# Kernel tuning notes

Measured on AMD Instinct MI355X. Metric: run time of the kernel, lower is better.

## Reference

```python
import jax, jax.numpy as jnp
import numpy as np

D_OUT = 32


def mlp(x, Ws, bs):
    # Ws: (L+1, d, d), bs: (L+1, d); relu after hidden layers, linear output
    h = x
    n = Ws.shape[0]
    for i in range(n - 1):
        h = jax.nn.relu(h @ Ws[i] + bs[i])
    return h @ Ws[n - 1] + bs[n - 1]


def causal_dot_product(Q, K, V, t1, t2):
    """out[:,:,i] = Q_i @ sum_{j: t2[j] <= t1[i]} K_j V_j^T.
    t2 is sorted (timestamps), so the cumulative outer-product state can be
    computed with a cumsum and gathered via searchsorted.
    Q: (1,1,T1,d); K,V: (1,1,T2,d); t1: (T1,); t2: (T2,).
    """
    outer = K[..., :, :, None] * V[..., :, None, :]      # (1,1,T2,d,d)
    S = jnp.cumsum(outer, axis=2)                        # prefix states
    idx = jnp.searchsorted(t2, t1, side='right') - 1     # (T1,)
    valid = idx >= 0
    Sg = S[:, :, jnp.maximum(idx, 0)]                    # (1,1,T1,d,d)
    out = jnp.einsum('bhid,bhide->bhie', Q, Sg)
    return jnp.where(valid[None, None, :, None], out, jnp.zeros((), out.dtype))


def _with_sorted_time(x, key):
    T = x.shape[2]
    t = jnp.sort(jax.random.uniform(key, (T,), dtype=jnp.float32)) * 100.0
    return x.at[0, 0, :, -1].set(t)


def setup_inputs() -> dict:
    key = jax.random.key(0)
    ks = jax.random.split(key, 16)
    d = 64
    Ts = [4096, 6144, 8192, 4096]
    mods = {}
    for i, T in enumerate(Ts):
        x = jax.random.normal(ks[i], (1, 1, T, d), dtype=jnp.float32)
        mods[f'm{i+1}'] = _with_sorted_time(x, ks[8 + i])
    scale = 1.0 / np.sqrt(d)
    WQ_w = jax.random.normal(ks[4], (3, d, d), dtype=jnp.float32) * scale
    WQ_b = jnp.zeros((3, d), dtype=jnp.float32)
    WK_w = jax.random.normal(ks[5], (4, 3, d, d), dtype=jnp.float32) * scale
    WK_b = jnp.zeros((4, 3, d), dtype=jnp.float32)
    return dict(m1=mods['m1'], m2=mods['m2'], m3=mods['m3'], m4=mods['m4'],
                WQ_w=WQ_w, WQ_b=WQ_b, WK_w=WK_w, WK_b=WK_b)


def reference(m1, m2, m3, m4, WQ_w, WQ_b, WK_w, WK_b):
    Q = mlp(m1, WQ_w, WQ_b)            # (1,1,T1,d)
    t1 = m1[0, 0, :, -1]               # (T1,)
    total = None
    for mi, X in enumerate([m1, m2, m3, m4]):
        K = mlp(X, WK_w[mi], WK_b[mi])
        V = X
        t2 = X[0, 0, :, -1]
        Z = causal_dot_product(Q, K, V, t1, t2)  # (1,1,T1,d)
        total = Z if total is None else total + Z
    # cat over dim=1 then sum(1) == sum of per-modality results, dim 1 dropped
    yhat = total.sum(axis=1)[..., :D_OUT]        # (1,T1,d_out)
    return yhat
```

## Files before the change

kernel.cpp:

```cpp
#include <hip/hip_runtime.h>


#define QB_OFF   0
#define KB_OFF   131072
#define SP_OFF   851968
#define TD_OFF   1581056
#define C_OFF    1603584

typedef __attribute__((ext_vector_type(8))) short short8;
typedef __attribute__((ext_vector_type(4))) float floatx4;

__device__ __forceinline__ unsigned short f2bf(float f) {
    union { float f; unsigned u; } v; v.f = f;
    unsigned r = v.u + 0x7fff + ((v.u >> 16) & 1);
    return (unsigned short)(r >> 16);
}

#define MFMA16(a,b,c) __builtin_amdgcn_mfma_f32_16x16x32_bf16((a),(b),(c),0,0,0)

__global__ __launch_bounds__(256) void k_fused(
    const float* __restrict__ x0, const float* __restrict__ x1,
    const float* __restrict__ x2, const float* __restrict__ x3,
    const float* __restrict__ wq_w, const float* __restrict__ wq_b,
    const float* __restrict__ wk_w, const float* __restrict__ wk_b,
    float* __restrict__ ws)
{
    __shared__ unsigned short H0[64*72];
    __shared__ unsigned short H1[64*72];
    __shared__ unsigned short Wt[3][64*72];
    __shared__ unsigned short KT[64*72];
    __shared__ unsigned short VT[32*72];

    const int tid = threadIdx.x;
    const int bid = blockIdx.x;

    int task, rb;
    if (bid < 64)       { task = 0; rb = bid; }
    else if (bid < 128) { task = 1; rb = bid - 64; }
    else if (bid < 224) { task = 2; rb = bid - 128; }
    else if (bid < 352) { task = 3; rb = bid - 224; }
    else                { task = 4; rb = bid - 352; }

    const float* Xs[4] = {x0, x1, x2, x3};
    const int rowoff[4] = {0, 4096, 10240, 18432};
    const int spoff[4]  = {0, 65, 162, 291};

    const float* X; const float* W; const float* Bv; int mm = -1;
    if (task == 0) { X = x0; W = wq_w; Bv = wq_b; }
    else {
        mm = task - 1;
        X = Xs[mm]; W = wk_w + mm*3*64*64; Bv = wk_b + mm*3*64;
    }

    const int row0 = rb * 64;

    {
        const float4* X4 = (const float4*)(X + (size_t)row0*64);
        #pragma unroll
        for (int k = 0; k < 4; ++k) {
            int idx = k*256 + tid;
            float4 v = X4[idx];
            int rr = idx >> 4, c4 = (idx & 15) * 4;
            ushort4 h;
            h.x = f2bf(v.x); h.y = f2bf(v.y); h.z = f2bf(v.z); h.w = f2bf(v.w);
            *(ushort4*)&H0[rr*72 + c4] = h;
        }
        const float4* W4 = (const float4*)W;
        #pragma unroll
        for (int k = 0; k < 12; ++k) {
            int idx = k*256 + tid;
            float4 v = W4[idx];
            int l = idx >> 10, rest = idx & 1023;
            int d = rest >> 4, c4 = (rest & 15) * 4;
            Wt[l][(c4+0)*72 + d] = f2bf(v.x);
            Wt[l][(c4+1)*72 + d] = f2bf(v.y);
            Wt[l][(c4+2)*72 + d] = f2bf(v.z);
            Wt[l][(c4+3)*72 + d] = f2bf(v.w);
        }
    }
    if (task > 0 && tid < 64)
        ws[TD_OFF + rowoff[mm] + row0 + tid] = X[(size_t)(row0 + tid)*64 + 63];
    __syncthreads();

    const int w    = tid >> 6;
    const int lane = tid & 63;
    const int lm   = lane & 15;
    const int q    = lane >> 4;
    const int col  = w*16 + lm;

    #pragma unroll 1
    for (int l = 0; l < 3; ++l) {
        const unsigned short* Hin  = (l & 1) ? H1 : H0;
        unsigned short*       Hout = (l & 1) ? H0 : H1;
        float bias = Bv[l*64 + col];
        short8 b0 = *(const short8*)&Wt[l][col*72 + q*8];
        short8 b1 = *(const short8*)&Wt[l][col*72 + 32 + q*8];
        #pragma unroll
        for (int mt = 0; mt < 4; ++mt) {
            floatx4 acc = {bias, bias, bias, bias};
            short8 a0 = *(const short8*)&Hin[(mt*16+lm)*72 + q*8];
            short8 a1 = *(const short8*)&Hin[(mt*16+lm)*72 + 32 + q*8];
            acc = MFMA16(a0, b0, acc);
            acc = MFMA16(a1, b1, acc);
            int r0 = mt*16 + q*4;
            #pragma unroll
            for (int r = 0; r < 4; ++r) {
                float f = acc[r];
                if (l < 2) f = fmaxf(f, 0.0f);
                unsigned short hb = f2bf(f);
                Hout[(r0+r)*72 + col] = hb;
                if (l == 2 && task > 0) KT[col*72 + r0 + r] = hb;
            }
        }
        __syncthreads();
    }

    {
        unsigned short* dst = (task == 0)
            ? (unsigned short*)(ws + QB_OFF)
            : (unsigned short*)(ws + KB_OFF) + (size_t)rowoff[mm]*64;
        #pragma unroll
        for (int k = 0; k < 4; ++k) {
            int idx = k*256 + tid;
            int rr = idx >> 4, c4 = (idx & 15) * 4;
            *(ushort4*)&dst[(size_t)(row0 + rr)*64 + c4] = *(ushort4*)&H1[rr*72 + c4];
        }
    }
    if (task == 0) return;

    {
        #pragma unroll
        for (int k = 0; k < 2; ++k) {
            int idx = k*256 + tid;
            int j = idx >> 3, e4 = (idx & 7) * 4;
            float4 v = *(const float4*)&X[(size_t)(row0 + j)*64 + e4];
            VT[(e4+0)*72 + j] = f2bf(v.x);
            VT[(e4+1)*72 + j] = f2bf(v.y);
            VT[(e4+2)*72 + j] = f2bf(v.z);
            VT[(e4+3)*72 + j] = f2bf(v.w);
        }
    }
    float* spbase = ws + SP_OFF + (size_t)spoff[mm]*2048;
    if (rb == 0)
        for (int idx = tid; idx < 2048; idx += 256) spbase[idx] = 0.0f;
    __syncthreads();

    {
        float* slot = spbase + (size_t)(rb + 1) * 2048;
        #pragma unroll
        for (int nt = 0; nt < 2; ++nt) {
            floatx4 acc = {0.f, 0.f, 0.f, 0.f};
            #pragma unroll
            for (int ks = 0; ks < 2; ++ks) {
                short8 aa = *(const short8*)&KT[col*72 + ks*32 + q*8];
                short8 bb = *(const short8*)&VT[(nt*16+lm)*72 + ks*32 + q*8];
                acc = MFMA16(aa, bb, acc);
            }
            #pragma unroll
            for (int r = 0; r < 4; ++r)
                slot[(w*16 + q*4 + r)*32 + nt*16 + lm] = acc[r];
        }
    }
}

__global__ __launch_bounds__(256) void k_prefix(float* __restrict__ ws,
                                                float* __restrict__ out)
{
    const int nslots[4] = {65, 97, 129, 65};
    const int spoff[4]  = {0, 65, 162, 291};
    const int Tm[4]     = {4096, 6144, 8192, 4096};
    const int rowoff[4] = {0, 4096, 10240, 18432};
    const int bid = blockIdx.x;
    const int tid = threadIdx.x;

    if (bid < 32) {
        int chain = bid*256 + tid;
        int m = chain >> 11, entry = chain & 2047;
        float* p = ws + SP_OFF + (size_t)spoff[m]*2048 + entry;
        const int n = nslots[m];
        float s = 0.0f;
        #pragma unroll 8
        for (int k = 0; k < n; ++k) {
            float v = p[(size_t)k*2048];
            s += v;
            p[(size_t)k*2048] = s;
        }
    } else if (bid < 34) {
        const float* td = ws + TD_OFF;
        int* ctab = (int*)(ws + C_OFF);
        int g = (bid - 32)*256 + tid;
        int m = g >> 7, tile = (g >> 1) & 63, bound = g & 1;
        float t = td[tile*64 + (bound ? 63 : 0)];
        const float* t2 = td + rowoff[m];
        int lo = 0, hi = Tm[m];
        while (lo < hi) {
            int mid = (lo + hi) >> 1;
            if (t2[mid] <= t) lo = mid + 1; else hi = mid;
        }
        ctab[g] = lo;
    } else {
        float4 z = make_float4(0.f, 0.f, 0.f, 0.f);
        #pragma unroll
        for (int k = 0; k < 16; ++k)
            ((float4*)out)[(bid - 34)*4096 + k*256 + tid] = z;
    }
}

__global__ __launch_bounds__(256) void k_query(
    const float* __restrict__ x0, const float* __restrict__ x1,
    const float* __restrict__ x2, const float* __restrict__ x3,
    float* __restrict__ ws, float* __restrict__ out)
{
    __shared__ unsigned short qs[64*72];
    __shared__ unsigned short kc[64*72];
    __shared__ unsigned short vt[32*72];
    __shared__ unsigned short st[32*72];
    __shared__ unsigned short ps[64*72];
    __shared__ float tq[64];
    __shared__ float tcs[64];

    const int tid  = threadIdx.x;
    const int m    = blockIdx.x & 3;
    const int tile = (blockIdx.x >> 2) & 63;
    const int slot = blockIdx.x >> 8;
    const int i0   = tile * 64;

    const float* Xs[4] = {x0, x1, x2, x3};
    const int rowoff[4] = {0, 4096, 10240, 18432};
    const int spoff[4]  = {0, 65, 162, 291};
    const float* X = Xs[m];

    const int* ctab = (const int*)(ws + C_OFF);
    const int c_lo = ctab[m*128 + tile*2 + 0];
    const int c_hi = ctab[m*128 + tile*2 + 1];
    const int B0   = c_lo >> 6;
    const int Bhi  = (c_hi + 63) >> 6;

    if (slot == 1 && B0 + 1 >= Bhi) return;

    const unsigned short* Qg = (const unsigned short*)(ws + QB_OFF);
    const unsigned short* Kg = (const unsigned short*)(ws + KB_OFF) + (size_t)rowoff[m]*64;
    const float* td = ws + TD_OFF;
    const float* sp = ws + SP_OFF + (size_t)(spoff[m] + B0)*2048;

    #pragma unroll
    for (int k = 0; k < 4; ++k) {
        int idx = k*256 + tid;
        int rr = idx >> 4, c4 = (idx & 15) * 4;
        *(ushort4*)&qs[rr*72 + c4] = *(const ushort4*)&Qg[(size_t)(i0 + rr)*64 + c4];
    }
    if (slot == 0) {
        #pragma unroll
        for (int k = 0; k < 8; ++k) {
            int idx = k*256 + tid;
            int d = idx >> 5, e = idx & 31;
            st[e*72 + d] = f2bf(sp[idx]);
        }
    }
    if (tid < 64) tq[tid] = td[i0 + tid];
    __syncthreads();

    const int w    = tid >> 6;
    const int lane = tid & 63;
    const int lm   = lane & 15;
    const int q    = lane >> 4;

    float t1v[16];
    #pragma unroll
    for (int mt = 0; mt < 4; ++mt)
        #pragma unroll
        for (int r = 0; r < 4; ++r)
            t1v[mt*4 + r] = tq[mt*16 + q*4 + r];

    short8 qa[4][2];
    #pragma unroll
    for (int mt = 0; mt < 4; ++mt) {
        qa[mt][0] = *(const short8*)&qs[(mt*16+lm)*72 + q*8];
        qa[mt][1] = *(const short8*)&qs[(mt*16+lm)*72 + 32 + q*8];
    }

    floatx4 accO[2];
    accO[0] = (floatx4){0.f, 0.f, 0.f, 0.f};
    accO[1] = (floatx4){0.f, 0.f, 0.f, 0.f};

    if (slot == 0) {
        #pragma unroll
        for (int nt = 0; nt < 2; ++nt) {
            #pragma unroll
            for (int ks = 0; ks < 2; ++ks) {
                short8 b = *(const short8*)&st[(nt*16+lm)*72 + ks*32 + q*8];
                accO[nt] = MFMA16(qa[w][ks], b, accO[nt]);
            }
        }
    }

    #pragma unroll 1
    for (int B = B0 + slot; B < Bhi; B += 2) {
        __syncthreads();
        #pragma unroll
        for (int k = 0; k < 4; ++k) {
            int idx = k*256 + tid;
            int j = idx >> 4, c4 = (idx & 15) * 4;
            *(ushort4*)&kc[j*72 + c4] = *(const ushort4*)&Kg[(size_t)(B*64 + j)*64 + c4];
        }
        #pragma unroll
        for (int k = 0; k < 2; ++k) {
            int idx = k*256 + tid;
            int j = idx >> 3, e4 = (idx & 7) * 4;
            float4 v = *(const float4*)&X[(size_t)(B*64 + j)*64 + e4];
            vt[(e4+0)*72 + j] = f2bf(v.x);
            vt[(e4+1)*72 + j] = f2bf(v.y);
            vt[(e4+2)*72 + j] = f2bf(v.z);
            vt[(e4+3)*72 + j] = f2bf(v.w);
        }
        if (tid < 64) tcs[tid] = td[rowoff[m] + B*64 + tid];
        __syncthreads();

        {
            short8 bk0 = *(const short8*)&kc[(w*16+lm)*72 + q*8];
            short8 bk1 = *(const short8*)&kc[(w*16+lm)*72 + 32 + q*8];
            float t2j = tcs[w*16 + lm];
            #pragma unroll
            for (int mt = 0; mt < 4; ++mt) {
                floatx4 f = {0.f, 0.f, 0.f, 0.f};
                f = MFMA16(qa[mt][0], bk0, f);
                f = MFMA16(qa[mt][1], bk1, f);
                #pragma unroll
                for (int r = 0; r < 4; ++r) {
                    float p = (t2j <= t1v[mt*4 + r]) ? f[r] : 0.0f;
                    ps[(mt*16 + q*4 + r)*72 + w*16 + lm] = f2bf(p);
                }
            }
        }
        __syncthreads();

        {
            short8 pa0 = *(const short8*)&ps[(w*16+lm)*72 + q*8];
            short8 pa1 = *(const short8*)&ps[(w*16+lm)*72 + 32 + q*8];
            #pragma unroll
            for (int nt = 0; nt < 2; ++nt) {
                short8 bv0 = *(const short8*)&vt[(nt*16+lm)*72 + q*8];
                short8 bv1 = *(const short8*)&vt[(nt*16+lm)*72 + 32 + q*8];
                accO[nt] = MFMA16(pa0, bv0, accO[nt]);
                accO[nt] = MFMA16(pa1, bv1, accO[nt]);
            }
        }
    }

    #pragma unroll
    for (int nt = 0; nt < 2; ++nt)
        #pragma unroll
        for (int r = 0; r < 4; ++r) {
            int i = w*16 + q*4 + r;
            int e = nt*16 + lm;
            atomicAdd(&out[(size_t)(i0 + i)*32 + e], accO[nt][r]);
        }
}

extern "C" void kernel_launch(void* const* d_in, const int* in_sizes, int n_in,
                              void* d_out, int out_size, void* d_ws, size_t ws_size,
                              hipStream_t stream) {
    const float* x0   = (const float*)d_in[0];
    const float* x1   = (const float*)d_in[1];
    const float* x2   = (const float*)d_in[2];
    const float* x3   = (const float*)d_in[3];
    const float* wq_w = (const float*)d_in[4];
    const float* wq_b = (const float*)d_in[5];
    const float* wk_w = (const float*)d_in[6];
    const float* wk_b = (const float*)d_in[7];
    float* ws  = (float*)d_ws;
    float* out = (float*)d_out;

    hipLaunchKernelGGL(k_fused,  dim3(416), dim3(256), 0, stream,
                       x0, x1, x2, x3, wq_w, wq_b, wk_w, wk_b, ws);
    hipLaunchKernelGGL(k_prefix, dim3(42),  dim3(256), 0, stream, ws, out);
    hipLaunchKernelGGL(k_query,  dim3(512), dim3(256), 0, stream,
                       x0, x1, x2, x3, ws, out);
}
```

Measured before the change: 107.3 us.

## Merge three kernels into one cooperative persistent kernel with grid syncs

Replaces the three separate launches (MLP plus chunk states, prefix scan, query) with a single cooperative kernel of 416 blocks that uses grid-wide syncs between phases. Work is redistributed: the prefix scan runs on 128 blocks split into quarters, the boundary search on two blocks, and the query tiles are looped over the persistent grid. This is meant to remove kernel launch gaps and tail effects between phases, at the cost of grid-sync overhead and a loop where 512 tiles over 416 blocks may leave load imbalance. It falls back to the old three-kernel path if the cooperative launch fails.

```diff
diff --git a/kernel.cpp b/kernel.cpp
--- a/kernel.cpp
+++ b/kernel.cpp
@@ -1,4 +1,7 @@
 #include <hip/hip_runtime.h>
+#include <hip/hip_cooperative_groups.h>
+
+namespace cg = cooperative_groups;
 
 
 #define QB_OFF   0
@@ -17,6 +20,344 @@
 }
 
 #define MFMA16(a,b,c) __builtin_amdgcn_mfma_f32_16x16x32_bf16((a),(b),(c),0,0,0)
+
+__global__ __launch_bounds__(256, 2) void k_all(
+    const float* __restrict__ x0, const float* __restrict__ x1,
+    const float* __restrict__ x2, const float* __restrict__ x3,
+    const float* __restrict__ wq_w, const float* __restrict__ wq_b,
+    const float* __restrict__ wk_w, const float* __restrict__ wk_b,
+    float* __restrict__ ws, float* __restrict__ out)
+{
+    __shared__ unsigned short SH[6*4608 + 2304];
+    __shared__ float SF[320];
+
+    const int tid = threadIdx.x;
+    const int bid = blockIdx.x;
+
+    const float* Xs[4] = {x0, x1, x2, x3};
+    const int rowoff[4] = {0, 4096, 10240, 18432};
+    const int spoff[4]  = {0, 65, 162, 291};
+    const int nslots[4] = {65, 97, 129, 65};
+    const int Tm[4]     = {4096, 6144, 8192, 4096};
+
+    const int w    = tid >> 6;
+    const int lane = tid & 63;
+    const int lm   = lane & 15;
+    const int q    = lane >> 4;
+    const int col  = w*16 + lm;
+
+    {
+        unsigned short* H0 = SH;
+        unsigned short* H1 = SH + 4608;
+        unsigned short* Wt = SH + 2*4608;
+        unsigned short* KT = SH + 5*4608;
+        unsigned short* VT = SH + 6*4608;
+
+        int task, rb;
+        if (bid < 64)       { task = 0; rb = bid; }
+        else if (bid < 128) { task = 1; rb = bid - 64; }
+        else if (bid < 224) { task = 2; rb = bid - 128; }
+        else if (bid < 352) { task = 3; rb = bid - 224; }
+        else                { task = 4; rb = bid - 352; }
+
+        const float* X; const float* W; const float* Bv; int mm = -1;
+        if (task == 0) { X = x0; W = wq_w; Bv = wq_b; }
+        else {
+            mm = task - 1;
+            X = Xs[mm]; W = wk_w + mm*3*64*64; Bv = wk_b + mm*3*64;
+        }
+
+        const int row0 = rb * 64;
+
+        {
+            const float4* X4 = (const float4*)(X + (size_t)row0*64);
+            #pragma unroll
+            for (int k = 0; k < 4; ++k) {
+                int idx = k*256 + tid;
+                float4 v = X4[idx];
+                int rr = idx >> 4, c4 = (idx & 15) * 4;
+                ushort4 h;
+                h.x = f2bf(v.x); h.y = f2bf(v.y); h.z = f2bf(v.z); h.w = f2bf(v.w);
+                *(ushort4*)&H0[rr*72 + c4] = h;
+            }
+            const float4* W4 = (const float4*)W;
+            #pragma unroll
+            for (int k = 0; k < 12; ++k) {
+                int idx = k*256 + tid;
+                float4 v = W4[idx];
+                int l = idx >> 10, rest = idx & 1023;
+                int d = rest >> 4, c4 = (rest & 15) * 4;
+                Wt[l*4608 + (c4+0)*72 + d] = f2bf(v.x);
+                Wt[l*4608 + (c4+1)*72 + d] = f2bf(v.y);
+                Wt[l*4608 + (c4+2)*72 + d] = f2bf(v.z);
+                Wt[l*4608 + (c4+3)*72 + d] = f2bf(v.w);
+            }
+        }
+        if (task == 0) {
+            float4 z = make_float4(0.f, 0.f, 0.f, 0.f);
+            ((float4*)out)[bid*512 + tid] = z;
+            ((float4*)out)[bid*512 + 256 + tid] = z;
+        }
+        if (task > 0 && tid < 64)
+            ws[TD_OFF + rowoff[mm] + row0 + tid] = X[(size_t)(row0 + tid)*64 + 63];
+        __syncthreads();
+
+        #pragma unroll 1
+        for (int l = 0; l < 3; ++l) {
+            const unsigned short* Hin  = (l & 1) ? H1 : H0;
+            unsigned short*       Hout = (l & 1) ? H0 : H1;
+            float bias = Bv[l*64 + col];
+            short8 b0 = *(const short8*)&Wt[l*4608 + col*72 + q*8];
+            short8 b1 = *(const short8*)&Wt[l*4608 + col*72 + 32 + q*8];
+            #pragma unroll
+            for (int mt = 0; mt < 4; ++mt) {
+                floatx4 acc = {bias, bias, bias, bias};
+                short8 a0 = *(const short8*)&Hin[(mt*16+lm)*72 + q*8];
+                short8 a1 = *(const short8*)&Hin[(mt*16+lm)*72 + 32 + q*8];
+                acc = MFMA16(a0, b0, acc);
+                acc = MFMA16(a1, b1, acc);
+                int r0 = mt*16 + q*4;
+                #pragma unroll
+                for (int r = 0; r < 4; ++r) {
+                    float f = acc[r];
+                    if (l < 2) f = fmaxf(f, 0.0f);
+                    unsigned short hb = f2bf(f);
+                    Hout[(r0+r)*72 + col] = hb;
+                    if (l == 2 && task > 0) KT[col*72 + r0 + r] = hb;
+                }
+            }
+            __syncthreads();
+        }
+
+        {
+            unsigned short* dst = (task == 0)
+                ? (unsigned short*)(ws + QB_OFF)
+                : (unsigned short*)(ws + KB_OFF) + (size_t)rowoff[mm]*64;
+            #pragma unroll
+            for (int k = 0; k < 4; ++k) {
+                int idx = k*256 + tid;
+                int rr = idx >> 4, c4 = (idx & 15) * 4;
+                *(ushort4*)&dst[(size_t)(row0 + rr)*64 + c4] = *(ushort4*)&H1[rr*72 + c4];
+            }
+        }
+
+        if (task > 0) {
+            #pragma unroll
+            for (int k = 0; k < 2; ++k) {
+                int idx = k*256 + tid;
+                int j = idx >> 3, e4 = (idx & 7) * 4;
+                float4 v = *(const float4*)&X[(size_t)(row0 + j)*64 + e4];
+                VT[(e4+0)*72 + j] = f2bf(v.x);
+                VT[(e4+1)*72 + j] = f2bf(v.y);
+                VT[(e4+2)*72 + j] = f2bf(v.z);
+                VT[(e4+3)*72 + j] = f2bf(v.w);
+            }
+            float* spbase = ws + SP_OFF + (size_t)spoff[mm]*2048;
+            if (rb == 0)
+                for (int idx = tid; idx < 2048; idx += 256) spbase[idx] = 0.0f;
+            __syncthreads();
+
+            float* slot = spbase + (size_t)(rb + 1) * 2048;
+            #pragma unroll
+            for (int nt = 0; nt < 2; ++nt) {
+                floatx4 acc = {0.f, 0.f, 0.f, 0.f};
+                #pragma unroll
+                for (int ks = 0; ks < 2; ++ks) {
+                    short8 aa = *(const short8*)&KT[col*72 + ks*32 + q*8];
+                    short8 bb = *(const short8*)&VT[(nt*16+lm)*72 + ks*32 + q*8];
+                    acc = MFMA16(aa, bb, acc);
+                }
+                #pragma unroll
+                for (int r = 0; r < 4; ++r)
+                    slot[(w*16 + q*4 + r)*32 + nt*16 + lm] = acc[r];
+            }
+        }
+    }
+
+    __threadfence();
+    cg::this_grid().sync();
+
+    if (bid < 128) {
+        const int m   = bid >> 5;
+        const int e   = tid & 63;
+        const int qtr = tid >> 6;
+        const int entry = (bid & 31)*64 + e;
+        const int n = nslots[m];
+        float* p = ws + SP_OFF + (size_t)spoff[m]*2048 + entry;
+        const int k0 = (qtr*n) >> 2;
+        const int k1 = ((qtr+1)*n) >> 2;
+        float s = 0.0f;
+        #pragma unroll 8
+        for (int k = k0; k < k1; ++k) s += p[(size_t)k*2048];
+        SF[qtr*64 + e] = s;
+        __syncthreads();
+        float base = 0.0f;
+        #pragma unroll
+        for (int q2 = 0; q2 < 3; ++q2) if (q2 < qtr) base += SF[q2*64 + e];
+        s = base;
+        #pragma unroll 8
+        for (int k = k0; k < k1; ++k) {
+            s += p[(size_t)k*2048];
+            p[(size_t)k*2048] = s;
+        }
+    } else if (bid < 130) {
+        const float* td = ws + TD_OFF;
+        int* ctab = (int*)(ws + C_OFF);
+        int g = (bid - 128)*256 + tid;
+        int m = g >> 7, tile = (g >> 1) & 63, bound = g & 1;
+        float t = td[tile*64 + (bound ? 63 : 0)];
+        const float* t2 = td + rowoff[m];
+        int lo = 0, hi = Tm[m];
+        while (lo < hi) {
+            int mid = (lo + hi) >> 1;
+            if (t2[mid] <= t) lo = mid + 1; else hi = mid;
+        }
+        ctab[g] = lo;
+    }
+
+    __threadfence();
+    cg::this_grid().sync();
+
+    {
+        unsigned short* qs = SH;
+        unsigned short* kc = SH + 4608;
+        unsigned short* ps = SH + 2*4608;
+        unsigned short* vt = SH + 3*4608;
+        unsigned short* st = SH + 3*4608 + 2304;
+        float* tq  = SF;
+        float* tcs = SF + 64;
+
+        for (int lb = bid; lb < 512; lb += 416) {
+            __syncthreads();
+            const int m    = lb & 3;
+            const int tile = (lb >> 2) & 63;
+            const int slot = lb >> 8;
+            const int i0   = tile * 64;
+            const float* X = Xs[m];
+
+            const int* ctab = (const int*)(ws + C_OFF);
+            const int c_lo = ctab[m*128 + tile*2 + 0];
+            const int c_hi = ctab[m*128 + tile*2 + 1];
+            const int B0   = c_lo >> 6;
+            const int Bhi  = (c_hi + 63) >> 6;
+
+            if (slot == 1 && B0 + 1 >= Bhi) continue;
+
+            const unsigned short* Qg = (const unsigned short*)(ws + QB_OFF);
+            const unsigned short* Kg = (const unsigned short*)(ws + KB_OFF) + (size_t)rowoff[m]*64;
+            const float* td = ws + TD_OFF;
+            const float* sp = ws + SP_OFF + (size_t)(spoff[m] + B0)*2048;
+
+            #pragma unroll
+            for (int k = 0; k < 4; ++k) {
+                int idx = k*256 + tid;
+                int rr = idx >> 4, c4 = (idx & 15) * 4;
+                *(ushort4*)&qs[rr*72 + c4] = *(const ushort4*)&Qg[(size_t)(i0 + rr)*64 + c4];
+            }
+            if (slot == 0) {
+                #pragma unroll
+                for (int k = 0; k < 8; ++k) {
+                    int idx = k*256 + tid;
+                    int d = idx >> 5, ee = idx & 31;
+                    st[ee*72 + d] = f2bf(sp[idx]);
+                }
+            }
+            if (tid < 64) tq[tid] = td[i0 + tid];
+            __syncthreads();
+
+            float t1v[16];
+            #pragma unroll
+            for (int mt = 0; mt < 4; ++mt)
+                #pragma unroll
+                for (int r = 0; r < 4; ++r)
+                    t1v[mt*4 + r] = tq[mt*16 + q*4 + r];
+
+            short8 qa[4][2];
+            #pragma unroll
+            for (int mt = 0; mt < 4; ++mt) {
+                qa[mt][0] = *(const short8*)&qs[(mt*16+lm)*72 + q*8];
+                qa[mt][1] = *(const short8*)&qs[(mt*16+lm)*72 + 32 + q*8];
+            }
+
+            floatx4 accO[2];
+            accO[0] = (floatx4){0.f, 0.f, 0.f, 0.f};
+            accO[1] = (floatx4){0.f, 0.f, 0.f, 0.f};
+
+            if (slot == 0) {
+                #pragma unroll
+                for (int nt = 0; nt < 2; ++nt) {
+                    #pragma unroll
+                    for (int ks = 0; ks < 2; ++ks) {
+                        short8 b = *(const short8*)&st[(nt*16+lm)*72 + ks*32 + q*8];
+                        accO[nt] = MFMA16(qa[w][ks], b, accO[nt]);
+                    }
+                }
+            }
+
+            #pragma unroll 1
+            for (int B = B0 + slot; B < Bhi; B += 2) {
+                __syncthreads();
+                #pragma unroll
+                for (int k = 0; k < 4; ++k) {
+                    int idx = k*256 + tid;
+                    int j = idx >> 4, c4 = (idx & 15) * 4;
+                    *(ushort4*)&kc[j*72 + c4] = *(const ushort4*)&Kg[(size_t)(B*64 + j)*64 + c4];
+                }
+                #pragma unroll
+                for (int k = 0; k < 2; ++k) {
+                    int idx = k*256 + tid;
+                    int j = idx >> 3, e4 = (idx & 7) * 4;
+                    float4 v = *(const float4*)&X[(size_t)(B*64 + j)*64 + e4];
+                    vt[(e4+0)*72 + j] = f2bf(v.x);
+                    vt[(e4+1)*72 + j] = f2bf(v.y);
+                    vt[(e4+2)*72 + j] = f2bf(v.z);
+                    vt[(e4+3)*72 + j] = f2bf(v.w);
+                }
+                if (tid < 64) tcs[tid] = td[rowoff[m] + B*64 + tid];
+                __syncthreads();
+
+                {
+                    short8 bk0 = *(const short8*)&kc[(w*16+lm)*72 + q*8];
+                    short8 bk1 = *(const short8*)&kc[(w*16+lm)*72 + 32 + q*8];
+                    float t2j = tcs[w*16 + lm];
+                    #pragma unroll
+                    for (int mt = 0; mt < 4; ++mt) {
+                        floatx4 f = {0.f, 0.f, 0.f, 0.f};
+                        f = MFMA16(qa[mt][0], bk0, f);
+                        f = MFMA16(qa[mt][1], bk1, f);
+                        #pragma unroll
+                        for (int r = 0; r < 4; ++r) {
+                            float pv = (t2j <= t1v[mt*4 + r]) ? f[r] : 0.0f;
+                            ps[(mt*16 + q*4 + r)*72 + w*16 + lm] = f2bf(pv);
+                        }
+                    }
+                }
+                __syncthreads();
+
+                {
+                    short8 pa0 = *(const short8*)&ps[(w*16+lm)*72 + q*8];
+                    short8 pa1 = *(const short8*)&ps[(w*16+lm)*72 + 32 + q*8];
+                    #pragma unroll
+                    for (int nt = 0; nt < 2; ++nt) {
+                        short8 bv0 = *(const short8*)&vt[(nt*16+lm)*72 + q*8];
+                        short8 bv1 = *(const short8*)&vt[(nt*16+lm)*72 + 32 + q*8];
+                        accO[nt] = MFMA16(pa0, bv0, accO[nt]);
+                        accO[nt] = MFMA16(pa1, bv1, accO[nt]);
+                    }
+                }
+            }
+
+            #pragma unroll
+            for (int nt = 0; nt < 2; ++nt)
+                #pragma unroll
+                for (int r = 0; r < 4; ++r) {
+                    int i = w*16 + q*4 + r;
+                    int e = nt*16 + lm;
+                    atomicAdd(&out[(size_t)(i0 + i)*32 + e], accO[nt][r]);
+                }
+        }
+    }
+}
 
 __global__ __launch_bounds__(256) void k_fused(
     const float* __restrict__ x0, const float* __restrict__ x1,
@@ -371,9 +712,20 @@
     float* ws  = (float*)d_ws;
     float* out = (float*)d_out;
 
-    hipLaunchKernelGGL(k_fused,  dim3(416), dim3(256), 0, stream,
-                       x0, x1, x2, x3, wq_w, wq_b, wk_w, wk_b, ws);
-    hipLaunchKernelGGL(k_prefix, dim3(42),  dim3(256), 0, stream, ws, out);
-    hipLaunchKernelGGL(k_query,  dim3(512), dim3(256), 0, stream,
-                       x0, x1, x2, x3, ws, out);
+    void* args[10] = {
+        (void*)&x0, (void*)&x1, (void*)&x2, (void*)&x3,
+        (void*)&wq_w, (void*)&wq_b, (void*)&wk_w, (void*)&wk_b,
+        (void*)&ws, (void*)&out
+    };
+    hipError_t rc = hipLaunchCooperativeKernel((const void*)k_all,
+                                               dim3(416), dim3(256),
+                                               args, 0, stream);
+    if (rc != hipSuccess) {
+        (void)hipGetLastError();
+        hipLaunchKernelGGL(k_fused,  dim3(416), dim3(256), 0, stream,
+                           x0, x1, x2, x3, wq_w, wq_b, wk_w, wk_b, ws);
+        hipLaunchKernelGGL(k_prefix, dim3(42),  dim3(256), 0, stream, ws, out);
+        hipLaunchKernelGGL(k_query,  dim3(512), dim3(256), 0, stream,
+                           x0, x1, x2, x3, ws, out);
+    }
 }
```

New measurement: 306.1 us. 185% more time.

## Remove prefix kernel: query blocks sum bf16 block states and search bounds inline

Applied to the files above, without the earlier changes.

Drops the separate prefix-scan kernel. Each query block now sums the needed per-block KV outer-product states directly, split across the two slot blocks, and finds its key-range bounds with a wave-wide ballot search. Block states are stored in bf16 to halve their traffic, and output zeroing moves into the first kernel. This removes a launch and a serial 129-step scan chain. In exchange every query block re-reads up to about 128 state slots, and bf16 partial states add rounding error.

```diff
diff --git a/kernel.cpp b/kernel.cpp
--- a/kernel.cpp
+++ b/kernel.cpp
@@ -5,7 +5,6 @@
 #define KB_OFF   131072
 #define SP_OFF   851968
 #define TD_OFF   1581056
-#define C_OFF    1603584
 
 typedef __attribute__((ext_vector_type(8))) short short8;
 typedef __attribute__((ext_vector_type(4))) float floatx4;
@@ -14,6 +13,10 @@
     union { float f; unsigned u; } v; v.f = f;
     unsigned r = v.u + 0x7fff + ((v.u >> 16) & 1);
     return (unsigned short)(r >> 16);
+}
+__device__ __forceinline__ float bf2f(unsigned short h) {
+    union { unsigned u; float f; } v; v.u = ((unsigned)h) << 16;
+    return v.f;
 }
 
 #define MFMA16(a,b,c) __builtin_amdgcn_mfma_f32_16x16x32_bf16((a),(b),(c),0,0,0)
@@ -23,7 +26,7 @@
     const float* __restrict__ x2, const float* __restrict__ x3,
     const float* __restrict__ wq_w, const float* __restrict__ wq_b,
     const float* __restrict__ wk_w, const float* __restrict__ wk_b,
-    float* __restrict__ ws)
+    float* __restrict__ ws, float* __restrict__ out)
 {
     __shared__ unsigned short H0[64*72];
     __shared__ unsigned short H1[64*72];
@@ -43,7 +46,7 @@
 
     const float* Xs[4] = {x0, x1, x2, x3};
     const int rowoff[4] = {0, 4096, 10240, 18432};
-    const int spoff[4]  = {0, 65, 162, 291};
+    const int spoffc[4] = {0, 64, 160, 288};
 
     const float* X; const float* W; const float* Bv; int mm = -1;
     if (task == 0) { X = x0; W = wq_w; Bv = wq_b; }
@@ -78,6 +81,11 @@
             Wt[l][(c4+3)*72 + d] = f2bf(v.w);
         }
     }
+    if (task == 0) {
+        float4 z = make_float4(0.f, 0.f, 0.f, 0.f);
+        ((float4*)out)[bid*512 + tid] = z;
+        ((float4*)out)[bid*512 + 256 + tid] = z;
+    }
     if (task > 0 && tid < 64)
         ws[TD_OFF + rowoff[mm] + row0 + tid] = X[(size_t)(row0 + tid)*64 + 63];
     __syncthreads();
@@ -140,13 +148,11 @@
             VT[(e4+3)*72 + j] = f2bf(v.w);
         }
     }
-    float* spbase = ws + SP_OFF + (size_t)spoff[mm]*2048;
-    if (rb == 0)
-        for (int idx = tid; idx < 2048; idx += 256) spbase[idx] = 0.0f;
     __syncthreads();
 
     {
-        float* slot = spbase + (size_t)(rb + 1) * 2048;
+        unsigned short* slotH = (unsigned short*)(ws + SP_OFF)
+                              + (size_t)(spoffc[mm] + rb) * 2048;
         #pragma unroll
         for (int nt = 0; nt < 2; ++nt) {
             floatx4 acc = {0.f, 0.f, 0.f, 0.f};
@@ -158,51 +164,8 @@
             }
             #pragma unroll
             for (int r = 0; r < 4; ++r)
-                slot[(w*16 + q*4 + r)*32 + nt*16 + lm] = acc[r];
-        }
-    }
-}
-
-__global__ __launch_bounds__(256) void k_prefix(float* __restrict__ ws,
-                                                float* __restrict__ out)
-{
-    const int nslots[4] = {65, 97, 129, 65};
-    const int spoff[4]  = {0, 65, 162, 291};
-    const int Tm[4]     = {4096, 6144, 8192, 4096};
-    const int rowoff[4] = {0, 4096, 10240, 18432};
-    const int bid = blockIdx.x;
-    const int tid = threadIdx.x;
-
-    if (bid < 32) {
-        int chain = bid*256 + tid;
-        int m = chain >> 11, entry = chain & 2047;
-        float* p = ws + SP_OFF + (size_t)spoff[m]*2048 + entry;
-        const int n = nslots[m];
-        float s = 0.0f;
-        #pragma unroll 8
-        for (int k = 0; k < n; ++k) {
-            float v = p[(size_t)k*2048];
-            s += v;
-            p[(size_t)k*2048] = s;
-        }
-    } else if (bid < 34) {
-        const float* td = ws + TD_OFF;
-        int* ctab = (int*)(ws + C_OFF);
-        int g = (bid - 32)*256 + tid;
-        int m = g >> 7, tile = (g >> 1) & 63, bound = g & 1;
-        float t = td[tile*64 + (bound ? 63 : 0)];
-        const float* t2 = td + rowoff[m];
-        int lo = 0, hi = Tm[m];
-        while (lo < hi) {
-            int mid = (lo + hi) >> 1;
-            if (t2[mid] <= t) lo = mid + 1; else hi = mid;
-        }
-        ctab[g] = lo;
-    } else {
-        float4 z = make_float4(0.f, 0.f, 0.f, 0.f);
-        #pragma unroll
-        for (int k = 0; k < 16; ++k)
-            ((float4*)out)[(bid - 34)*4096 + k*256 + tid] = z;
+                slotH[(w*16 + q*4 + r)*32 + nt*16 + lm] = f2bf(acc[r]);
+        }
     }
 }
 
@@ -218,6 +181,7 @@
     __shared__ unsigned short ps[64*72];
     __shared__ float tq[64];
     __shared__ float tcs[64];
+    __shared__ int   SB[2];
 
     const int tid  = threadIdx.x;
     const int m    = blockIdx.x & 3;
@@ -225,23 +189,21 @@
     const int slot = blockIdx.x >> 8;
     const int i0   = tile * 64;
 
+    const int w    = tid >> 6;
+    const int lane = tid & 63;
+    const int lm   = lane & 15;
+    const int q    = lane >> 4;
+
     const float* Xs[4] = {x0, x1, x2, x3};
     const int rowoff[4] = {0, 4096, 10240, 18432};
-    const int spoff[4]  = {0, 65, 162, 291};
+    const int spoffc[4] = {0, 64, 160, 288};
+    const int Tm[4]     = {4096, 6144, 8192, 4096};
     const float* X = Xs[m];
 
-    const int* ctab = (const int*)(ws + C_OFF);
-    const int c_lo = ctab[m*128 + tile*2 + 0];
-    const int c_hi = ctab[m*128 + tile*2 + 1];
-    const int B0   = c_lo >> 6;
-    const int Bhi  = (c_hi + 63) >> 6;
-
-    if (slot == 1 && B0 + 1 >= Bhi) return;
-
-    const unsigned short* Qg = (const unsigned short*)(ws + QB_OFF);
-    const unsigned short* Kg = (const unsigned short*)(ws + KB_OFF) + (size_t)rowoff[m]*64;
+    const unsigned short* Qg  = (const unsigned short*)(ws + QB_OFF);
+    const unsigned short* Kg  = (const unsigned short*)(ws + KB_OFF) + (size_t)rowoff[m]*64;
+    const unsigned short* SPH = (const unsigned short*)(ws + SP_OFF);
     const float* td = ws + TD_OFF;
-    const float* sp = ws + SP_OFF + (size_t)(spoff[m] + B0)*2048;
 
     #pragma unroll
     for (int k = 0; k < 4; ++k) {
@@ -249,21 +211,55 @@
         int rr = idx >> 4, c4 = (idx & 15) * 4;
         *(ushort4*)&qs[rr*72 + c4] = *(const ushort4*)&Qg[(size_t)(i0 + rr)*64 + c4];
     }
-    if (slot == 0) {
-        #pragma unroll
-        for (int k = 0; k < 8; ++k) {
-            int idx = k*256 + tid;
-            int d = idx >> 5, e = idx & 31;
-            st[e*72 + d] = f2bf(sp[idx]);
-        }
-    }
     if (tid < 64) tq[tid] = td[i0 + tid];
+
+    if (w < 2) {
+        float t = td[i0 + (w ? 63 : 0)];
+        const float* t2 = td + rowoff[m];
+        int lo = 0, hi = Tm[m];
+        while (hi - lo > 64) {
+            int step = (hi - lo + 63) >> 6;
+            int pos = lo + lane*step;
+            bool pred = (pos < hi) && (t2[pos] <= t);
+            int c = __popcll(__ballot(pred));
+            int nhi = (c < 64) ? (lo + c*step) : hi;
+            if (nhi > hi) nhi = hi;
+            if (c) lo = lo + (c-1)*step + 1;
+            hi = nhi;
+        }
+        int pos = lo + lane;
+        bool pred = (pos < hi) && (t2[pos] <= t);
+        int c = __popcll(__ballot(pred));
+        if (lane == 0) SB[w] = lo + c;
+    }
     __syncthreads();
 
-    const int w    = tid >> 6;
-    const int lane = tid & 63;
-    const int lm   = lane & 15;
-    const int q    = lane >> 4;
+    const int c_lo = SB[0];
+    const int c_hi = SB[1];
+    const int B0   = c_lo >> 6;
+    const int Bhi  = (c_hi + 63) >> 6;
+
+    {
+        float sacc[8] = {0.f,0.f,0.f,0.f,0.f,0.f,0.f,0.f};
+        const unsigned short* sp0 = SPH + (size_t)spoffc[m]*2048 + tid*8;
+        #pragma unroll 2
+        for (int k = slot; k < B0; k += 2) {
+            uint4 pv = *(const uint4*)(sp0 + (size_t)k*2048);
+            sacc[0] += bf2f((unsigned short)(pv.x & 0xffffu));
+            sacc[1] += bf2f((unsigned short)(pv.x >> 16));
+            sacc[2] += bf2f((unsigned short)(pv.y & 0xffffu));
+            sacc[3] += bf2f((unsigned short)(pv.y >> 16));
+            sacc[4] += bf2f((unsigned short)(pv.z & 0xffffu));
+            sacc[5] += bf2f((unsigned short)(pv.z >> 16));
+            sacc[6] += bf2f((unsigned short)(pv.w & 0xffffu));
+            sacc[7] += bf2f((unsigned short)(pv.w >> 16));
+        }
+        int d0 = (tid*8) >> 5, e0 = (tid*8) & 31;
+        #pragma unroll
+        for (int k = 0; k < 8; ++k)
+            st[(e0+k)*72 + d0] = f2bf(sacc[k]);
+    }
+    __syncthreads();
 
     float t1v[16];
     #pragma unroll
@@ -283,14 +279,12 @@
     accO[0] = (floatx4){0.f, 0.f, 0.f, 0.f};
     accO[1] = (floatx4){0.f, 0.f, 0.f, 0.f};
 
-    if (slot == 0) {
-        #pragma unroll
-        for (int nt = 0; nt < 2; ++nt) {
-            #pragma unroll
-            for (int ks = 0; ks < 2; ++ks) {
-                short8 b = *(const short8*)&st[(nt*16+lm)*72 + ks*32 + q*8];
-                accO[nt] = MFMA16(qa[w][ks], b, accO[nt]);
-            }
+    #pragma unroll
+    for (int nt = 0; nt < 2; ++nt) {
+        #pragma unroll
+        for (int ks = 0; ks < 2; ++ks) {
+            short8 b = *(const short8*)&st[(nt*16+lm)*72 + ks*32 + q*8];
+            accO[nt] = MFMA16(qa[w][ks], b, accO[nt]);
         }
     }
 
@@ -371,9 +365,8 @@
     float* ws  = (float*)d_ws;
     float* out = (float*)d_out;
 
-    hipLaunchKernelGGL(k_fused,  dim3(416), dim3(256), 0, stream,
-                       x0, x1, x2, x3, wq_w, wq_b, wk_w, wk_b, ws);
-    hipLaunchKernelGGL(k_prefix, dim3(42),  dim3(256), 0, stream, ws, out);
-    hipLaunchKernelGGL(k_query,  dim3(512), dim3(256), 0, stream,
+    hipLaunchKernelGGL(k_fused, dim3(416), dim3(256), 0, stream,
+                       x0, x1, x2, x3, wq_w, wq_b, wk_w, wk_b, ws, out);
+    hipLaunchKernelGGL(k_query, dim3(512), dim3(256), 0, stream,
                        x0, x1, x2, x3, ws, out);
 }
```

After: 105.9 us. No clear change (-1.4%).
